# Performance work log

Measured on AMD Instinct MI355X. Metric: run time of the kernel, lower is better.

## Reference

```python
import jax, jax.numpy as jnp
import numpy as np

H = 56; W = 56; WS = 7; SS = 3; HEADS = 12; DIM = 384
N = WS * WS; NW = (H // WS) * (W // WS); EPS = 1e-5


def _attn_mask():
    img = np.zeros((H, W), np.float32)
    cnt = 0
    for hs in (slice(0, -WS), slice(-WS, -SS), slice(-SS, None)):
        for ws in (slice(0, -WS), slice(-WS, -SS), slice(-SS, None)):
            img[hs, ws] = cnt
            cnt += 1
    m = img.reshape(H // WS, WS, W // WS, WS).transpose(0, 2, 1, 3).reshape(-1, N)
    d = m[:, None, :] - m[:, :, None]
    return jnp.asarray(np.where(d != 0, -100.0, 0.0).astype(np.float32))


def _rel_coords():
    c = np.stack(np.meshgrid(np.arange(WS), np.arange(WS), indexing='ij')).reshape(2, -1)
    rel = (c[:, :, None] - c[:, None, :]).astype(np.float32)
    rel = np.sign(rel) * np.log1p(np.abs(rel))
    return jnp.asarray(np.stack([rel[0], rel[1]], -1).reshape(-1, 2))


ATTN_MASK = _attn_mask()  # (NW, N, N)
REL = _rel_coords()       # (N*N, 2)


def _ln(x, g, b):
    mu = x.mean(-1, keepdims=True)
    var = ((x - mu) ** 2).mean(-1, keepdims=True)
    return (x - mu) / jnp.sqrt(var + EPS) * g + b


def setup_inputs() -> dict:
    key = jax.random.key(0)
    ks = jax.random.split(key, 8)
    s = 0.02
    B = 32
    return {
        'x': jax.random.normal(ks[0], (B, H * W, DIM), jnp.float32),
        'norm1_g': jnp.ones((DIM,), jnp.float32),
        'norm1_b': jnp.zeros((DIM,), jnp.float32),
        'qkv_w': jax.random.normal(ks[1], (DIM, 3 * DIM), jnp.float32) * s,
        'qkv_b': jnp.zeros((3 * DIM,), jnp.float32),
        'tau': jnp.ones((HEADS,), jnp.float32),
        'proj_w': jax.random.normal(ks[2], (DIM, DIM), jnp.float32) * s,
        'proj_b': jnp.zeros((DIM,), jnp.float32),
        'crpb_w1': jax.random.normal(ks[3], (2, 64), jnp.float32) * s,
        'crpb_b1': jnp.zeros((64,), jnp.float32),
        'crpb_w2': jax.random.normal(ks[4], (64, HEADS), jnp.float32) * s,
        'crpb_b2': jnp.zeros((HEADS,), jnp.float32),
        'norm2_g': jnp.ones((DIM,), jnp.float32),
        'norm2_b': jnp.zeros((DIM,), jnp.float32),
        'mlp_w1': jax.random.normal(ks[5], (DIM, 4 * DIM), jnp.float32) * s,
        'mlp_b1': jnp.zeros((4 * DIM,), jnp.float32),
        'mlp_w2': jax.random.normal(ks[6], (4 * DIM, DIM), jnp.float32) * s,
        'mlp_b2': jnp.zeros((DIM,), jnp.float32),
    }


def reference(x, norm1_g, norm1_b, qkv_w, qkv_b, tau, proj_w, proj_b,
              crpb_w1, crpb_b1, crpb_w2, crpb_b2, norm2_g, norm2_b,
              mlp_w1, mlp_b1, mlp_w2, mlp_b2):
    B = x.shape[0]
    shortcut = x
    h = _ln(x, norm1_g, norm1_b).reshape(B, H, W, DIM)
    # cyclic shift
    h = jnp.roll(h, (-SS, -SS), axis=(1, 2))
    # window partition -> (B*NW, N, DIM)
    xw = h.reshape(B, H // WS, WS, W // WS, WS, DIM).transpose(0, 1, 3, 2, 4, 5).reshape(-1, N, DIM)
    qkv = xw @ qkv_w + qkv_b
    q, k, v = jnp.split(qkv, 3, axis=-1)
    hd = DIM // HEADS
    def to_heads(t):
        return t.reshape(-1, N, HEADS, hd).transpose(0, 2, 1, 3)  # (Bw, heads, N, hd)
    q, k, v = to_heads(q), to_heads(k), to_heads(v)
    q = q / jnp.maximum(jnp.linalg.norm(q, axis=-1, keepdims=True), 1e-12)
    k = k / jnp.maximum(jnp.linalg.norm(k, axis=-1, keepdims=True), 1e-12)
    attn = jnp.einsum('whnd,whmd->whnm', q, k) * tau[None, :, None, None]
    # continuous relative position bias
    bias = jax.nn.relu(REL @ crpb_w1 + crpb_b1) @ crpb_w2 + crpb_b2  # (N*N, heads)
    bias = bias.reshape(N, N, HEADS).transpose(2, 0, 1)
    attn = attn + bias[None]
    attn = attn.reshape(B, NW, HEADS, N, N) + ATTN_MASK[None, :, None]
    attn = jax.nn.softmax(attn.reshape(-1, HEADS, N, N), axis=-1)
    out = jnp.einsum('whnm,whmd->whnd', attn, v).transpose(0, 2, 1, 3).reshape(-1, N, DIM)
    out = out @ proj_w + proj_b
    # window reverse
    h = out.reshape(B, H // WS, W // WS, WS, WS, DIM).transpose(0, 1, 3, 2, 4, 5).reshape(B, H, W, DIM)
    h = jnp.roll(h, (SS, SS), axis=(1, 2)).reshape(B, H * W, DIM)
    x = shortcut + h
    m = _ln(x, norm2_g, norm2_b)
    m = jax.nn.gelu(m @ mlp_w1 + mlp_b1, approximate=False) @ mlp_w2 + mlp_b2
    return x + m
```

## Files before the change

kernel.cpp:

```cpp
#include <hip/hip_runtime.h>
#include <cstdint>
#include <cstddef>


typedef unsigned short u16;
typedef __bf16 bf16x8 __attribute__((ext_vector_type(8)));
typedef float f32x4 __attribute__((ext_vector_type(4)));

#define VMW8 asm volatile("s_waitcnt vmcnt(8)" ::: "memory")
#define VMW4 asm volatile("s_waitcnt vmcnt(4)" ::: "memory")
#define VMW0 asm volatile("s_waitcnt vmcnt(0)" ::: "memory")
#define LGKM0 asm volatile("s_waitcnt lgkmcnt(0)" ::: "memory")
#define BAR asm volatile("s_barrier" ::: "memory")

__device__ __forceinline__ u16 f2bf(float f) {
  unsigned u = __builtin_bit_cast(unsigned, f);
  u += 0x7fffu + ((u >> 16) & 1u);
  return (u16)(u >> 16);
}

__device__ __forceinline__ void gll16(const u16* g, u16* l) {
  __builtin_amdgcn_global_load_lds(
      (const __attribute__((address_space(1))) void*)g,
      (__attribute__((address_space(3))) void*)l, 16, 0, 0);
}

__global__ __launch_bounds__(256) void fill_k(float* o, int n) {
  int i = blockIdx.x * 256 + threadIdx.x;
  if (i < n) o[i] = 12345.0f;
}

__global__ __launch_bounds__(256) void wconv_k(
    const float* __restrict__ qkv_w, const float* __restrict__ proj_w,
    const float* __restrict__ mlp_w1, const float* __restrict__ mlp_w2,
    u16* __restrict__ o) {
  const int id = blockIdx.x * 256 + threadIdx.x;
  if (id < 442368) {
    const int n = id / 384, k = id - n * 384;
    o[id] = f2bf(qkv_w[k * 1152 + n]);
  } else if (id < 589824) {
    const int e = id - 442368; const int n = e / 384, k = e - n * 384;
    o[id] = f2bf(proj_w[k * 384 + n]);
  } else if (id < 1179648) {
    const int e = id - 589824; const int n = e / 384, k = e - n * 384;
    o[id] = f2bf(mlp_w1[k * 1536 + n]);
  } else {
    const int e = id - 1179648; const int n = e / 1536, k = e - n * 1536;
    o[id] = f2bf(mlp_w2[k * 384 + n]);
  }
}

__global__ __launch_bounds__(256) void biastab_k(
    const float* __restrict__ w1, const float* __restrict__ b1,
    const float* __restrict__ w2, const float* __restrict__ b2,
    float* __restrict__ biasT) {
  const int id = blockIdx.x * 256 + threadIdx.x;
  if (id >= 2401) return;
  const int i = id / 49, j = id - i * 49;
  const int r1 = i / 7, c1 = i - r1 * 7, r2 = j / 7, c2 = j - r2 * 7;
  float dy = (float)(r1 - r2), dx = (float)(c1 - c2);
  dy = copysignf(log1pf(fabsf(dy)), dy);
  dx = copysignf(log1pf(fabsf(dx)), dx);
  float accv[12];
#pragma unroll
  for (int t = 0; t < 12; ++t) accv[t] = b2[t];
  for (int u = 0; u < 64; ++u) {
    float hu = fmaxf(dy * w1[u] + dx * w1[64 + u] + b1[u], 0.0f);
#pragma unroll
    for (int t = 0; t < 12; ++t) accv[t] += hu * w2[u * 12 + t];
  }
#pragma unroll
  for (int t = 0; t < 12; ++t) biasT[t * 2401 + id] = accv[t];
}

template <int WINMAP>
__global__ __launch_bounds__(256, 4) void ln_k(
    const float* __restrict__ X, const float* __restrict__ g,
    const float* __restrict__ b, u16* __restrict__ O) {
  const int t = blockIdx.x * 4 + (threadIdx.x >> 6);
  const int lane = threadIdx.x & 63;
  const float* xr = X + (size_t)t * 384;
  float v[6];
  float s = 0.f;
#pragma unroll
  for (int i = 0; i < 6; ++i) { v[i] = xr[lane + i * 64]; s += v[i]; }
#pragma unroll
  for (int m = 1; m < 64; m <<= 1) s += __shfl_xor(s, m);
  const float mu = s * (1.0f / 384.0f);
  float q = 0.f;
#pragma unroll
  for (int i = 0; i < 6; ++i) { float d = v[i] - mu; q += d * d; }
#pragma unroll
  for (int m = 1; m < 64; m <<= 1) q += __shfl_xor(q, m);
  const float rstd = rsqrtf(q * (1.0f / 384.0f) + 1e-5f);
  size_t row;
  if constexpr (WINMAP) {
    const int bb = t / 3136, hw = t - bb * 3136;
    const int ho = hw / 56, wo = hw - ho * 56;
    int hs = ho - 3; if (hs < 0) hs += 56;
    int ws2 = wo - 3; if (ws2 < 0) ws2 += 56;
    const int h7 = hs / 7, w7 = ws2 / 7;
    const int wwin = bb * 64 + h7 * 8 + w7;
    const int p = (hs - h7 * 7) * 7 + (ws2 - w7 * 7);
    row = (size_t)wwin * 49 + p;
  } else {
    row = (size_t)t;
  }
  u16* orow = O + row * 384;
#pragma unroll
  for (int i = 0; i < 6; ++i) {
    const int d = lane + i * 64;
    orow[d] = f2bf((v[i] - mu) * rstd * g[d] + b[d]);
  }
}

template <int EPI, int KK>
__global__ __launch_bounds__(256, 3) void gemm_k(
    const u16* __restrict__ A, const u16* __restrict__ Bt,
    const float* __restrict__ bias, const float* __restrict__ aux,
    void* __restrict__ outp, int M, int N) {
  __shared__ u16 Ab[3][4096];
  __shared__ u16 Bb[3][4096];
  const int tid = threadIdx.x;
  const int lane = tid & 63;
  const int wv = tid >> 6;
  const int wrow = wv >> 1, wcol = wv & 1;
  const int l15 = lane & 15, l4 = lane >> 4;

  const int nx = gridDim.x;
  const int nwg = nx * gridDim.y;
  int bid = blockIdx.y * nx + blockIdx.x;
  bid = (bid & 7) * (nwg >> 3) + (bid >> 3);
  const int tileN = (bid % nx) * 128;
  const int tileM = (bid / nx) * 128;

  const int prow = lane >> 2;
  const int lrow = prow ^ ((prow >> 2) & 1);
  const int lslot = (lane & 3) ^ (lrow & 3);
  const u16* Ag = A + (size_t)(tileM + wv * 16 + lrow) * KK + lslot * 8;
  const u16* Bg = Bt + (size_t)(tileN + wv * 16 + lrow) * KK + lslot * 8;
  const size_t skip = (size_t)64 * KK;

  f32x4 acc[4][4] = {};

#define STAGE(t, b)                                       \
  {                                                       \
    const size_t ko = (size_t)(t) * 32;                   \
    gll16(Ag + ko, &Ab[b][wv * 512]);                     \
    gll16(Ag + skip + ko, &Ab[b][(4 + wv) * 512]);        \
    gll16(Bg + ko, &Bb[b][wv * 512]);                     \
    gll16(Bg + skip + ko, &Bb[b][(4 + wv) * 512]);        \
  }

#define COMPUTE(b)                                                        \
  {                                                                       \
    bf16x8 af[4], bfr[4];                                                 \
    _Pragma("unroll") for (int f = 0; f < 4; ++f) {                       \
      const int Ra = wrow * 64 + f * 16 + l15;                            \
      const int Rb = wcol * 64 + f * 16 + l15;                            \
      af[f] = *(const bf16x8*)&Ab[b][(Ra * 32 + 8 * l4) ^ ((Ra & 7) << 3)];\
      bfr[f] = *(const bf16x8*)&Bb[b][(Rb * 32 + 8 * l4) ^ ((Rb & 7) << 3)];\
    }                                                                     \
    __builtin_amdgcn_s_setprio(1);                                        \
    _Pragma("unroll") for (int fm = 0; fm < 4; ++fm)                      \
        _Pragma("unroll") for (int fn = 0; fn < 4; ++fn) acc[fm][fn] =    \
            __builtin_amdgcn_mfma_f32_16x16x32_bf16(af[fm], bfr[fn],      \
                                                    acc[fm][fn], 0, 0, 0);\
    __builtin_amdgcn_s_setprio(0);                                        \
  }

  constexpr int nt = KK >> 5;
  STAGE(0, 0);
  STAGE(1, 1);
  int cur = 0, nxt = 2;
#pragma unroll 3
  for (int t = 0; t < nt - 2; ++t) {
    STAGE(t + 2, nxt);
    VMW8;
    BAR;
    COMPUTE(cur);
    BAR;
    cur = (cur == 2) ? 0 : cur + 1;
    nxt = (nxt == 2) ? 0 : nxt + 1;
  }
  VMW4;
  BAR;
  COMPUTE(cur);
  cur = (cur == 2) ? 0 : cur + 1;
  VMW0;
  BAR;
  COMPUTE(cur);
#undef STAGE
#undef COMPUTE

  const int baseRow = tileM + wrow * 64;
  const int baseCol = tileN + wcol * 64;

  if constexpr (EPI == 0) {
    u16* O = (u16*)outp;
#pragma unroll
    for (int fm = 0; fm < 4; ++fm) {
#pragma unroll
      for (int hp = 0; hp < 2; ++hp) {
        const int c0e = baseCol + hp * 32;
        const int seg = c0e >> 5;
        const bool nrm = seg < 24;
        const float tfac = (seg < 12) ? aux[seg] : 1.0f;
        const float b0 = bias[c0e + l15];
        const float b1 = bias[c0e + 16 + l15];
#pragma unroll
        for (int r = 0; r < 4; ++r) {
          float v0 = acc[fm][2 * hp][r] + b0;
          float v1 = acc[fm][2 * hp + 1][r] + b1;
          if (nrm) {
            float ss = v0 * v0 + v1 * v1;
            ss += __shfl_xor(ss, 1);
            ss += __shfl_xor(ss, 2);
            ss += __shfl_xor(ss, 4);
            ss += __shfl_xor(ss, 8);
            const float f = tfac / fmaxf(sqrtf(ss), 1e-12f);
            v0 *= f; v1 *= f;
          }
          const size_t row = (size_t)(baseRow + fm * 16 + l4 * 4 + r);
          O[row * N + c0e + l15] = f2bf(v0);
          O[row * N + c0e + 16 + l15] = f2bf(v1);
        }
      }
    }
  } else if constexpr (EPI == 1) {
    float* O = (float*)outp;
    const float* X = aux;
#pragma unroll
    for (int fm = 0; fm < 4; ++fm) {
#pragma unroll
      for (int r = 0; r < 4; ++r) {
        const int row = baseRow + fm * 16 + l4 * 4 + r;
        const int w = row / 49, p = row - w * 49;
        const int bb = w >> 6, widx = w & 63;
        const int p7 = p / 7;
        int hs = (widx >> 3) * 7 + p7;
        int ws2 = (widx & 7) * 7 + (p - p7 * 7);
        int ho = hs + 3; if (ho >= 56) ho -= 56;
        int wo = ws2 + 3; if (wo >= 56) wo -= 56;
        const size_t tok = (size_t)bb * 3136 + ho * 56 + wo;
#pragma unroll
        for (int fn = 0; fn < 4; ++fn) {
          const int col = baseCol + fn * 16 + l15;
          O[tok * 384 + col] = X[tok * 384 + col] + acc[fm][fn][r] + bias[col];
        }
      }
    }
  } else if constexpr (EPI == 2) {
    u16* O = (u16*)outp;
#pragma unroll
    for (int fm = 0; fm < 4; ++fm) {
#pragma unroll
      for (int fn = 0; fn < 4; ++fn) {
        const int col = baseCol + fn * 16 + l15;
        const float bc = bias[col];
#pragma unroll
        for (int r = 0; r < 4; ++r) {
          const size_t row = (size_t)(baseRow + fm * 16 + l4 * 4 + r);
          const float v = acc[fm][fn][r] + bc;
          const float g = 0.5f * v * (1.0f + erff(v * 0.70710678118654752f));
          O[row * N + col] = f2bf(g);
        }
      }
    }
  } else {
    float* O = (float*)outp;
#pragma unroll
    for (int fm = 0; fm < 4; ++fm) {
#pragma unroll
      for (int fn = 0; fn < 4; ++fn) {
        const int col = baseCol + fn * 16 + l15;
        const float bc = bias[col];
#pragma unroll
        for (int r = 0; r < 4; ++r) {
          const size_t row = (size_t)(baseRow + fm * 16 + l4 * 4 + r);
          O[row * N + col] += acc[fm][fn][r] + bc;
        }
      }
    }
  }
}

__global__ __launch_bounds__(256, 2) void attn_k(
    const u16* __restrict__ qkv, const float* __restrict__ biasT,
    u16* __restrict__ outp) {
  __shared__ u16 lds[4][7552];
  const int tid = threadIdx.x, lane = tid & 63, wid = tid >> 6;
  const int l15 = lane & 15, l4 = lane >> 4;
  const int W = blockIdx.x * 4 + wid;
  const int w = W / 12, h = W - w * 12;
  u16* S = lds[wid];
  u16* Q = S;
  u16* Kl = S + 2560;
  u16* P = S;
  u16* VT = S + 5120;
  float* sums = (float*)(S + 7424);
  const u16* base = qkv + (size_t)w * 56448 + h * 32;
  const int widx = w & 63, wh = widx >> 3, ww = widx & 7;
  const bool masked = (wh == 7) || (ww == 7);

#pragma unroll
  for (int it = 0; it < 4; ++it) {
    const int row = it * 16 + (lane >> 2);
    const int c8 = (lane & 3) * 8;
    uint4 qv = {0, 0, 0, 0}, kv = {0, 0, 0, 0};
    if (row < 49) {
      qv = *(const uint4*)(base + (size_t)row * 1152 + c8);
      kv = *(const uint4*)(base + (size_t)row * 1152 + 384 + c8);
    }
    *(uint4*)&Q[row * 40 + c8] = qv;
    *(uint4*)&Kl[row * 40 + c8] = kv;
  }
  {
    const int d = lane & 31;
    const int jh = lane >> 5;
#pragma unroll 4
    for (int jt = 0; jt < 32; ++jt) {
      const int j = jt * 2 + jh;
      u16 val = 0;
      if (j < 49) val = base[(size_t)j * 1152 + 768 + d];
      VT[d * 72 + j] = val;
    }
  }
  LGKM0;

  f32x4 sc[4][4] = {};
  {
    bf16x8 aq[4], bk[4];
#pragma unroll
    for (int f = 0; f < 4; ++f)
      aq[f] = *(const bf16x8*)&Q[(f * 16 + l15) * 40 + 8 * l4];
#pragma unroll
    for (int f = 0; f < 4; ++f)
      bk[f] = *(const bf16x8*)&Kl[(f * 16 + l15) * 40 + 8 * l4];
    __builtin_amdgcn_s_setprio(1);
#pragma unroll
    for (int fm = 0; fm < 4; ++fm)
#pragma unroll
      for (int fn = 0; fn < 4; ++fn)
        sc[fm][fn] = __builtin_amdgcn_mfma_f32_16x16x32_bf16(
            aq[fm], bk[fn], sc[fm][fn], 0, 0, 0);
    __builtin_amdgcn_s_setprio(0);
  }
  LGKM0;

  int codej[4] = {0, 0, 0, 0};
  if (masked) {
#pragma unroll
    for (int fn = 0; fn < 4; ++fn) {
      const int j = fn * 16 + l15;
      const int pr = j / 7, pc = j - pr * 7;
      const int rr2 = (wh == 7) ? ((pr < 4) ? 1 : 2) : 0;
      const int cc2 = (ww == 7) ? ((pc < 4) ? 1 : 2) : 0;
      codej[fn] = rr2 * 3 + cc2;
    }
  }
#pragma unroll
  for (int fm = 0; fm < 4; ++fm) {
#pragma unroll
    for (int r = 0; r < 4; ++r) {
      const int i = fm * 16 + l4 * 4 + r;
      const bool iok = i < 49;
      int ci = 0;
      if (masked && iok) {
        const int pr = i / 7, pc = i - pr * 7;
        const int rr2 = (wh == 7) ? ((pr < 4) ? 1 : 2) : 0;
        const int cc2 = (ww == 7) ? ((pc < 4) ? 1 : 2) : 0;
        ci = rr2 * 3 + cc2;
      }
      const float* brow = biasT + (size_t)h * 2401 + (iok ? i : 0) * 49;
      float sv[4];
#pragma unroll
      for (int fn = 0; fn < 4; ++fn) {
        const int j = fn * 16 + l15;
        float s = sc[fm][fn][r];
        if (iok && j < 49) {
          s += brow[j];
          if (masked && codej[fn] != ci) s -= 100.0f;
        } else {
          s = -1e30f;
        }
        sv[fn] = s;
      }
      float mx = fmaxf(fmaxf(sv[0], sv[1]), fmaxf(sv[2], sv[3]));
      mx = fmaxf(mx, __shfl_xor(mx, 1));
      mx = fmaxf(mx, __shfl_xor(mx, 2));
      mx = fmaxf(mx, __shfl_xor(mx, 4));
      mx = fmaxf(mx, __shfl_xor(mx, 8));
      float sm = 0.f;
      u16 pb[4];
#pragma unroll
      for (int fn = 0; fn < 4; ++fn) {
        const float e = __expf(sv[fn] - mx);
        sm += e;
        pb[fn] = f2bf(e);
      }
      sm += __shfl_xor(sm, 1);
      sm += __shfl_xor(sm, 2);
      sm += __shfl_xor(sm, 4);
      sm += __shfl_xor(sm, 8);
#pragma unroll
      for (int fn = 0; fn < 4; ++fn) P[i * 72 + fn * 16 + l15] = pb[fn];
      if (l15 == 0) sums[i] = sm;
    }
  }
  LGKM0;

  f32x4 o[4][2] = {};
#pragma unroll
  for (int kk = 0; kk < 2; ++kk) {
    bf16x8 pa[4], bv[2];
#pragma unroll
    for (int fm = 0; fm < 4; ++fm)
      pa[fm] = *(const bf16x8*)&P[(fm * 16 + l15) * 72 + kk * 32 + 8 * l4];
#pragma unroll
    for (int fn = 0; fn < 2; ++fn)
      bv[fn] = *(const bf16x8*)&VT[(fn * 16 + l15) * 72 + kk * 32 + 8 * l4];
    __builtin_amdgcn_s_setprio(1);
#pragma unroll
    for (int fm = 0; fm < 4; ++fm)
#pragma unroll
      for (int fn = 0; fn < 2; ++fn)
        o[fm][fn] = __builtin_amdgcn_mfma_f32_16x16x32_bf16(
            pa[fm], bv[fn], o[fm][fn], 0, 0, 0);
    __builtin_amdgcn_s_setprio(0);
  }
  u16* ob = outp + (size_t)w * 49 * 384 + h * 32;
#pragma unroll
  for (int fm = 0; fm < 4; ++fm) {
#pragma unroll
    for (int r = 0; r < 4; ++r) {
      const int i = fm * 16 + l4 * 4 + r;
      if (i < 49) {
        const float inv = 1.0f / sums[i];
        ob[(size_t)i * 384 + l15] = f2bf(o[fm][0][r] * inv);
        ob[(size_t)i * 384 + 16 + l15] = f2bf(o[fm][1][r] * inv);
      }
    }
  }
}

extern "C" void kernel_launch(void* const* d_in, const int* in_sizes, int n_in,
                              void* d_out, int out_size, void* d_ws,
                              size_t ws_size, hipStream_t stream) {
  const float* x      = (const float*)d_in[0];
  const float* n1g    = (const float*)d_in[1];
  const float* n1b    = (const float*)d_in[2];
  const float* qkv_w  = (const float*)d_in[3];
  const float* qkv_b  = (const float*)d_in[4];
  const float* tau    = (const float*)d_in[5];
  const float* proj_w = (const float*)d_in[6];
  const float* proj_b = (const float*)d_in[7];
  const float* c_w1   = (const float*)d_in[8];
  const float* c_b1   = (const float*)d_in[9];
  const float* c_w2   = (const float*)d_in[10];
  const float* c_b2   = (const float*)d_in[11];
  const float* n2g    = (const float*)d_in[12];
  const float* n2b    = (const float*)d_in[13];
  const float* mlp_w1 = (const float*)d_in[14];
  const float* mlp_b1 = (const float*)d_in[15];
  const float* mlp_w2 = (const float*)d_in[16];
  const float* mlp_b2 = (const float*)d_in[17];
  float* out = (float*)d_out;
  char* ws = (char*)d_ws;

  constexpr size_t WS_WT    = 0;
  constexpr size_t WS_BIAST = 3538944;
  constexpr size_t WS_XW    = 4194304;
  constexpr size_t WS_QKV   = 81264640;
  constexpr size_t WS_ATT   = 312475648;
  constexpr size_t WS_NEED  = 389545984;

  if (ws_size < WS_NEED) {
    fill_k<<<(out_size + 255) / 256, 256, 0, stream>>>(out, out_size);
    return;
  }

  u16* wqkvT  = (u16*)(ws + WS_WT);
  u16* wprojT = (u16*)(ws + WS_WT + 884736);
  u16* wm1T   = (u16*)(ws + WS_WT + 1179648);
  u16* wm2T   = (u16*)(ws + WS_WT + 2359296);
  float* biasT = (float*)(ws + WS_BIAST);
  u16* xw  = (u16*)(ws + WS_XW);
  u16* qkv = (u16*)(ws + WS_QKV);
  u16* att = (u16*)(ws + WS_ATT);
  u16* hid = qkv;
  u16* ln2 = xw;

  wconv_k<<<6912, 256, 0, stream>>>(qkv_w, proj_w, mlp_w1, mlp_w2, (u16*)ws);
  biastab_k<<<10, 256, 0, stream>>>(c_w1, c_b1, c_w2, c_b2, biasT);
  ln_k<1><<<25088, 256, 0, stream>>>(x, n1g, n1b, xw);
  gemm_k<0, 384><<<dim3(9, 784), 256, 0, stream>>>(xw, wqkvT, qkv_b, tau, qkv,
                                                   100352, 1152);
  attn_k<<<6144, 256, 0, stream>>>(qkv, biasT, att);
  gemm_k<1, 384><<<dim3(3, 784), 256, 0, stream>>>(att, wprojT, proj_b, x, out,
                                                   100352, 384);
  ln_k<0><<<25088, 256, 0, stream>>>(out, n2g, n2b, ln2);
  gemm_k<2, 384><<<dim3(12, 784), 256, 0, stream>>>(ln2, wm1T, mlp_b1, nullptr,
                                                    hid, 100352, 1536);
  gemm_k<3, 1536><<<dim3(3, 784), 256, 0, stream>>>(hid, wm2T, mlp_b2, nullptr,
                                                    out, 100352, 384);
}
```

Baseline: 1.427 ms.

## Load GEMM B operand directly from global into registers, single-buffer A in LDS

Replaces the triple-buffered global->LDS pipeline for both operands with a single LDS buffer for A and direct per-lane global loads of B fragments into registers. Occupancy hint goes from 3 to 4 blocks per CU to exploit the reduced LDS footprint. This removes the multi-stage prefetch, so global load latency is no longer overlapped with MFMA work and each K step now has two block-wide barriers. B fragment loads are also redundant across the two wave rows.

```diff
diff --git a/kernel.cpp b/kernel.cpp
--- a/kernel.cpp
+++ b/kernel.cpp
@@ -6,12 +6,6 @@
 typedef unsigned short u16;
 typedef __bf16 bf16x8 __attribute__((ext_vector_type(8)));
 typedef float f32x4 __attribute__((ext_vector_type(4)));
-
-#define VMW8 asm volatile("s_waitcnt vmcnt(8)" ::: "memory")
-#define VMW4 asm volatile("s_waitcnt vmcnt(4)" ::: "memory")
-#define VMW0 asm volatile("s_waitcnt vmcnt(0)" ::: "memory")
-#define LGKM0 asm volatile("s_waitcnt lgkmcnt(0)" ::: "memory")
-#define BAR asm volatile("s_barrier" ::: "memory")
 
 __device__ __forceinline__ u16 f2bf(float f) {
   unsigned u = __builtin_bit_cast(unsigned, f);
@@ -24,6 +18,8 @@
       (const __attribute__((address_space(1))) void*)g,
       (__attribute__((address_space(3))) void*)l, 16, 0, 0);
 }
+
+#define LGKM0 asm volatile("s_waitcnt lgkmcnt(0)" ::: "memory")
 
 __global__ __launch_bounds__(256) void fill_k(float* o, int n) {
   int i = blockIdx.x * 256 + threadIdx.x;
@@ -115,12 +111,11 @@
 }
 
 template <int EPI, int KK>
-__global__ __launch_bounds__(256, 3) void gemm_k(
+__global__ __launch_bounds__(256, 4) void gemm_k(
     const u16* __restrict__ A, const u16* __restrict__ Bt,
     const float* __restrict__ bias, const float* __restrict__ aux,
     void* __restrict__ outp, int M, int N) {
-  __shared__ u16 Ab[3][4096];
-  __shared__ u16 Bb[3][4096];
+  __shared__ u16 Ab[4096];
   const int tid = threadIdx.x;
   const int lane = tid & 63;
   const int wv = tid >> 6;
@@ -138,60 +133,40 @@
   const int lrow = prow ^ ((prow >> 2) & 1);
   const int lslot = (lane & 3) ^ (lrow & 3);
   const u16* Ag = A + (size_t)(tileM + wv * 16 + lrow) * KK + lslot * 8;
-  const u16* Bg = Bt + (size_t)(tileN + wv * 16 + lrow) * KK + lslot * 8;
   const size_t skip = (size_t)64 * KK;
 
+  const u16* Bgf[4];
+#pragma unroll
+  for (int f = 0; f < 4; ++f)
+    Bgf[f] = Bt + (size_t)(tileN + wcol * 64 + f * 16 + l15) * KK + 8 * l4;
+
   f32x4 acc[4][4] = {};
 
-#define STAGE(t, b)                                       \
-  {                                                       \
-    const size_t ko = (size_t)(t) * 32;                   \
-    gll16(Ag + ko, &Ab[b][wv * 512]);                     \
-    gll16(Ag + skip + ko, &Ab[b][(4 + wv) * 512]);        \
-    gll16(Bg + ko, &Bb[b][wv * 512]);                     \
-    gll16(Bg + skip + ko, &Bb[b][(4 + wv) * 512]);        \
-  }
-
-#define COMPUTE(b)                                                        \
-  {                                                                       \
-    bf16x8 af[4], bfr[4];                                                 \
-    _Pragma("unroll") for (int f = 0; f < 4; ++f) {                       \
-      const int Ra = wrow * 64 + f * 16 + l15;                            \
-      const int Rb = wcol * 64 + f * 16 + l15;                            \
-      af[f] = *(const bf16x8*)&Ab[b][(Ra * 32 + 8 * l4) ^ ((Ra & 7) << 3)];\
-      bfr[f] = *(const bf16x8*)&Bb[b][(Rb * 32 + 8 * l4) ^ ((Rb & 7) << 3)];\
-    }                                                                     \
-    __builtin_amdgcn_s_setprio(1);                                        \
-    _Pragma("unroll") for (int fm = 0; fm < 4; ++fm)                      \
-        _Pragma("unroll") for (int fn = 0; fn < 4; ++fn) acc[fm][fn] =    \
-            __builtin_amdgcn_mfma_f32_16x16x32_bf16(af[fm], bfr[fn],      \
-                                                    acc[fm][fn], 0, 0, 0);\
-    __builtin_amdgcn_s_setprio(0);                                        \
-  }
-
   constexpr int nt = KK >> 5;
-  STAGE(0, 0);
-  STAGE(1, 1);
-  int cur = 0, nxt = 2;
-#pragma unroll 3
-  for (int t = 0; t < nt - 2; ++t) {
-    STAGE(t + 2, nxt);
-    VMW8;
-    BAR;
-    COMPUTE(cur);
-    BAR;
-    cur = (cur == 2) ? 0 : cur + 1;
-    nxt = (nxt == 2) ? 0 : nxt + 1;
-  }
-  VMW4;
-  BAR;
-  COMPUTE(cur);
-  cur = (cur == 2) ? 0 : cur + 1;
-  VMW0;
-  BAR;
-  COMPUTE(cur);
-#undef STAGE
-#undef COMPUTE
+  for (int t = 0; t < nt; ++t) {
+    uint4 bv[4];
+#pragma unroll
+    for (int f = 0; f < 4; ++f)
+      bv[f] = *(const uint4*)(Bgf[f] + (size_t)t * 32);
+    __syncthreads();
+    gll16(Ag + (size_t)t * 32, &Ab[wv * 512]);
+    gll16(Ag + skip + (size_t)t * 32, &Ab[(4 + wv) * 512]);
+    __syncthreads();
+    bf16x8 af[4];
+#pragma unroll
+    for (int f = 0; f < 4; ++f) {
+      const int Ra = wrow * 64 + f * 16 + l15;
+      af[f] = *(const bf16x8*)&Ab[(Ra * 32 + 8 * l4) ^ ((Ra & 7) << 3)];
+    }
+    __builtin_amdgcn_s_setprio(1);
+#pragma unroll
+    for (int fm = 0; fm < 4; ++fm)
+#pragma unroll
+      for (int fn = 0; fn < 4; ++fn)
+        acc[fm][fn] = __builtin_amdgcn_mfma_f32_16x16x32_bf16(
+            af[fm], __builtin_bit_cast(bf16x8, bv[fn]), acc[fm][fn], 0, 0, 0);
+    __builtin_amdgcn_s_setprio(0);
+  }
 
   const int baseRow = tileM + wrow * 64;
   const int baseCol = tileN + wcol * 64;
```

After: 1.624 ms. 13.8% more time.
